# Kernel optimization log

Measured on AMD Instinct MI355X. Metric: run time of the kernel, lower is better.

Reference implementation:

```python
import jax, jax.numpy as jnp
import numpy as np

N_NODES = 100000
N_EDGES = 1600000
IN_C = 128
HID_C = 128   # 2 * out_channels
OUT_C = 64


def gcn_conv(x, row, col, w, W, b, num_nodes):
    """PyG GCNConv: linear transform, add self-loops (weight 1),
    symmetric degree normalization, scatter-sum aggregation, bias."""
    h = x @ W  # [N, C_out]
    loop = jnp.arange(num_nodes, dtype=row.dtype)
    r = jnp.concatenate([row, loop])
    c = jnp.concatenate([col, loop])
    ew = jnp.concatenate([w, jnp.ones((num_nodes,), dtype=w.dtype)])
    deg = jax.ops.segment_sum(ew, c, num_segments=num_nodes)
    dinv = jnp.where(deg > 0, jax.lax.rsqrt(deg), 0.0)
    norm = dinv[r] * ew * dinv[c]            # [E+N]
    msg = h[r] * norm[:, None]               # [E+N, C_out] gather
    out = jax.ops.segment_sum(msg, c, num_segments=num_nodes)
    return out + b


def setup_inputs() -> dict:
    key = jax.random.key(0)
    k1, k2, k3, k4, k5, k6, k7, k8 = jax.random.split(key, 8)
    x = jax.random.normal(k1, (N_NODES, IN_C), dtype=jnp.float32)
    edge_index = jax.random.randint(k2, (2, N_EDGES), 0, N_NODES, dtype=jnp.int64)
    edge_weight = jax.random.uniform(k3, (N_EDGES,), dtype=jnp.float32)
    s1 = float(np.sqrt(6.0 / (IN_C + HID_C)))
    s2 = float(np.sqrt(6.0 / (HID_C + OUT_C)))
    W1 = jax.random.uniform(k4, (IN_C, HID_C), minval=-s1, maxval=s1, dtype=jnp.float32)
    b1 = jnp.zeros((HID_C,), dtype=jnp.float32)
    W2 = jax.random.uniform(k5, (HID_C, OUT_C), minval=-s2, maxval=s2, dtype=jnp.float32)
    b2 = jnp.zeros((OUT_C,), dtype=jnp.float32)
    return {"x": x, "edge_index": edge_index, "edge_weight": edge_weight,
            "W1": W1, "b1": b1, "W2": W2, "b2": b2}


def reference(x, edge_index, edge_weight, W1, b1, W2, b2):
    row, col = edge_index[0], edge_index[1]
    n = x.shape[0]
    h = jax.nn.relu(gcn_conv(x, row, col, edge_weight, W1, b1, n))
    h = jax.nn.relu(gcn_conv(h, row, col, edge_weight, W2, b2, n))
    return h
```

## Files before the change

kernel.cpp:

```cpp
#include <hip/hip_runtime.h>

#define TPB 256

typedef unsigned int uint32;
typedef unsigned short ushort_t;
typedef __attribute__((ext_vector_type(8))) short bf16x8;
typedef __attribute__((ext_vector_type(4))) float f32x4;

constexpr int NB = 256;
constexpr int B1 = 256;

__device__ __forceinline__ uint32 pack_bf16x2(float a, float b) {
  uint32 ua = __float_as_uint(a), ub = __float_as_uint(b);
  ua += 0x7FFFu + ((ua >> 16) & 1u);
  ub += 0x7FFFu + ((ub >> 16) & 1u);
  return (ua >> 16) | (ub & 0xFFFF0000u);
}
__device__ __forceinline__ ushort_t bf16_of(float a) {
  uint32 u = __float_as_uint(a);
  u += 0x7FFFu + ((u >> 16) & 1u);
  return (ushort_t)(u >> 16);
}
__device__ __forceinline__ float bf16_lo(uint32 u) { return __uint_as_float(u << 16); }
__device__ __forceinline__ float bf16_hi(uint32 u) { return __uint_as_float(u & 0xFFFF0000u); }

__global__ __launch_bounds__(256) void rx_hist(const int* __restrict__ col,
                                               int* __restrict__ blockhist, int e, int chunk) {
  __shared__ int h[NB];
  int tid = threadIdx.x, blk = blockIdx.x;
  h[tid] = 0;
  __syncthreads();
  int s = blk * chunk, t = min(e, s + chunk);
  for (int i = s + tid; i < t; i += 256) atomicAdd(&h[col[i] & 255], 1);
  __syncthreads();
  blockhist[tid * B1 + blk] = h[tid];
}

__global__ __launch_bounds__(256) void k_scan1(int* __restrict__ a, int* __restrict__ bsum, int n) {
  __shared__ int s[256];
  int tid = threadIdx.x;
  int base = blockIdx.x * 1024 + tid * 4;
  int v0 = 0, v1 = 0, v2 = 0, v3 = 0;
  if (base + 0 < n) v0 = a[base + 0];
  if (base + 1 < n) v1 = a[base + 1];
  if (base + 2 < n) v2 = a[base + 2];
  if (base + 3 < n) v3 = a[base + 3];
  int tsum = v0 + v1 + v2 + v3;
  s[tid] = tsum;
  __syncthreads();
  for (int off = 1; off < 256; off <<= 1) {
    int t = (tid >= off) ? s[tid - off] : 0;
    __syncthreads();
    s[tid] += t;
    __syncthreads();
  }
  if (tid == 255) bsum[blockIdx.x] = s[255];
  int e0 = s[tid] - tsum;
  int e1 = e0 + v0, e2 = e1 + v1, e3 = e2 + v2;
  if (base + 0 < n) a[base + 0] = e0;
  if (base + 1 < n) a[base + 1] = e1;
  if (base + 2 < n) a[base + 2] = e2;
  if (base + 3 < n) a[base + 3] = e3;
}

__global__ __launch_bounds__(256) void k_scan2(int* __restrict__ bsum, int nb) {
  __shared__ int s[256];
  int tid = threadIdx.x;
  int v = (tid < nb) ? bsum[tid] : 0;
  s[tid] = v;
  __syncthreads();
  for (int off = 1; off < 256; off <<= 1) {
    int t = (tid >= off) ? s[tid - off] : 0;
    __syncthreads();
    s[tid] += t;
    __syncthreads();
  }
  if (tid < nb) bsum[tid] = s[tid] - v;
}

__global__ void k_scan3b(int* __restrict__ a, const int* __restrict__ bsum, int n) {
  int i = blockIdx.x * TPB + threadIdx.x;
  if (i < n) a[i] += bsum[i >> 10];
}

__global__ __launch_bounds__(256) void rx_scatter1(const int* __restrict__ row,
                                                   const int* __restrict__ col,
                                                   const float* __restrict__ w,
                                                   const int* __restrict__ scanned,
                                                   int2* __restrict__ rec, int e, int chunk) {
  __shared__ int cur[NB];
  int tid = threadIdx.x, blk = blockIdx.x;
  cur[tid] = scanned[tid * B1 + blk];
  __syncthreads();
  int s = blk * chunk, t = min(e, s + chunk);
  for (int i = s + tid; i < t; i += 256) {
    int c = col[i];
    int p = atomicAdd(&cur[c & 255], 1);
    rec[p] = make_int2(row[i] | ((c >> 8) << 20), __float_as_int(w[i]));
  }
}

__global__ __launch_bounds__(256) void rx_build(const int2* __restrict__ rec,
                                                const int* __restrict__ scanned,
                                                int2* __restrict__ nodeRange,
                                                float* __restrict__ dinv,
                                                int2* __restrict__ edges, int n, int e) {
  constexpr int NH = 512;
  __shared__ int cnt[NH];
  __shared__ int pref[NH];
  __shared__ int cur[NH];
  __shared__ float dw[NH];
  __shared__ int ssum[256];
  int tid = threadIdx.x, lo = blockIdx.x;
  int s = scanned[lo * B1];
  int t = (lo == NB - 1) ? e : scanned[(lo + 1) * B1];
  cnt[tid] = 0; cnt[tid + 256] = 0;
  dw[tid] = 0.f; dw[tid + 256] = 0.f;
  __syncthreads();
  for (int i = s + tid; i < t; i += 256) {
    int2 r = rec[i];
    int hi = ((uint32)r.x) >> 20;
    atomicAdd(&cnt[hi], 1);
    atomicAdd(&dw[hi], __int_as_float(r.y));
  }
  __syncthreads();
  int a0 = cnt[2 * tid], a1 = cnt[2 * tid + 1];
  int sum2 = a0 + a1;
  ssum[tid] = sum2;
  __syncthreads();
  for (int off = 1; off < 256; off <<= 1) {
    int v = (tid >= off) ? ssum[tid - off] : 0;
    __syncthreads();
    ssum[tid] += v;
    __syncthreads();
  }
  int excl = ssum[tid] - sum2;
  pref[2 * tid] = excl;
  pref[2 * tid + 1] = excl + a0;
  __syncthreads();
#pragma unroll
  for (int k = 0; k < 2; ++k) {
    int hi = tid + k * 256;
    int node = (hi << 8) | lo;
    cur[hi] = s + pref[hi];
    if (node < n) {
      nodeRange[node] = make_int2(s + pref[hi], cnt[hi]);
      dinv[node] = rsqrtf(1.0f + dw[hi]);
    }
  }
  __syncthreads();
  for (int i = s + tid; i < t; i += 256) {
    int2 r = rec[i];
    int hi = ((uint32)r.x) >> 20;
    int p = atomicAdd(&cur[hi], 1);
    edges[p] = make_int2(r.x & 0xFFFFF, r.y);
  }
}

__global__ void k_wprep2(const float* __restrict__ W1, ushort_t* __restrict__ Wt1,
                         const float* __restrict__ W2, ushort_t* __restrict__ Wt2) {
  int i = blockIdx.x * TPB + threadIdx.x;
  if (i < 128 * 128) {
    int k = i >> 7, m = i & 127;
    Wt1[m * 128 + k] = bf16_of(W1[i]);
  } else {
    int j = i - 128 * 128;
    if (j < 128 * 64) {
      int k = j >> 6, m = j & 63;
      Wt2[m * 128 + k] = bf16_of(W2[j]);
    }
  }
}

template <int M, bool XF32>
__global__ __launch_bounds__(256) void k_gemm_mfma(
    const void* __restrict__ Xv, const ushort_t* __restrict__ Wt,
    const float* __restrict__ dinv, uint32* __restrict__ Hb, int n) {
  __shared__ __align__(16) char smem[16384 + M * 256];
  char* Xs = smem;
  char* Ws = smem + 16384;
  const int tid = threadIdx.x;
  const int lane = tid & 63;
  const int w = tid >> 6;
  const int row0 = blockIdx.x * 64;

  {
    const uint4* src = (const uint4*)Wt;
    for (int idx = tid; idx < M * 16; idx += 256) {
      int r = idx >> 4, g = idx & 15;
      uint4 v = src[idx];
      *(uint4*)(Ws + ((r << 8) | ((g << 4) ^ ((r & 7) << 4)))) = v;
    }
  }
  if constexpr (XF32) {
    const float4* src = (const float4*)Xv;
    for (int idx = tid; idx < 64 * 16; idx += 256) {
      int r = idx >> 4, g = idx & 15;
      int grow = row0 + r;
      float4 va = make_float4(0.f, 0.f, 0.f, 0.f), vb = va;
      if (grow < n) {
        va = src[(size_t)grow * 32 + g * 2];
        vb = src[(size_t)grow * 32 + g * 2 + 1];
      }
      uint4 p;
      p.x = pack_bf16x2(va.x, va.y);
      p.y = pack_bf16x2(va.z, va.w);
      p.z = pack_bf16x2(vb.x, vb.y);
      p.w = pack_bf16x2(vb.z, vb.w);
      *(uint4*)(Xs + ((r << 8) | ((g << 4) ^ ((r & 7) << 4)))) = p;
    }
  } else {
    const uint4* src = (const uint4*)Xv;
    for (int idx = tid; idx < 64 * 16; idx += 256) {
      int r = idx >> 4, g = idx & 15;
      int grow = row0 + r;
      uint4 v = make_uint4(0u, 0u, 0u, 0u);
      if (grow < n) v = src[(size_t)grow * 16 + g];
      *(uint4*)(Xs + ((r << 8) | ((g << 4) ^ ((r & 7) << 4)))) = v;
    }
  }
  __syncthreads();

  constexpr int CT = M / 16;
  f32x4 acc[CT];
#pragma unroll
  for (int c = 0; c < CT; ++c) acc[c] = (f32x4){0.f, 0.f, 0.f, 0.f};

  const int arow = (w << 4) | (lane & 15);
  const int kb0 = (lane >> 4) << 4;
#pragma unroll
  for (int ks = 0; ks < 4; ++ks) {
    int kbyte = ks * 64 + kb0;
    bf16x8 a = *(const bf16x8*)(Xs + ((arow << 8) | (kbyte ^ ((arow & 7) << 4))));
#pragma unroll
    for (int c = 0; c < CT; ++c) {
      int brow = c * 16 + (lane & 15);
      bf16x8 b = *(const bf16x8*)(Ws + ((brow << 8) | (kbyte ^ ((brow & 7) << 4))));
      acc[c] = __builtin_amdgcn_mfma_f32_16x16x32_bf16(a, b, acc[c], 0, 0, 0);
    }
  }
  __syncthreads();

  ushort_t* Cs = (ushort_t*)smem;
  const int rbase = (w << 4) | ((lane >> 4) << 2);
  float dv[4];
#pragma unroll
  for (int r = 0; r < 4; ++r) {
    int g = row0 + rbase + r;
    dv[r] = (g < n) ? dinv[g] : 0.f;
  }
#pragma unroll
  for (int c = 0; c < CT; ++c) {
    int col = c * 16 + (lane & 15);
#pragma unroll
    for (int r = 0; r < 4; ++r)
      Cs[(rbase + r) * 132 + col] = bf16_of(acc[c][r] * dv[r]);
  }
  __syncthreads();
  constexpr int G2 = M / 4;
  uint2* dst = (uint2*)Hb;
  for (int idx = tid; idx < 64 * G2; idx += 256) {
    int r = idx / G2, g = idx % G2;
    int grow = row0 + r;
    if (grow < n)
      dst[(size_t)grow * G2 + g] = *(const uint2*)((const char*)Cs + r * 264 + g * 8);
  }
}

template <int C>
__global__ __launch_bounds__(TPB) void k_agg(
    const uint32* __restrict__ hsb, const int2* __restrict__ edges,
    const int2* __restrict__ nodeRange, const float* __restrict__ dinv,
    const float* __restrict__ bias, void* __restrict__ out, int n) {
  int node = (blockIdx.x * TPB + threadIdx.x) >> 6;
  if (node >= n) return;
  int lane = threadIdx.x & 63;
  int g = lane >> 4;
  int gl = lane & 15;
  int2 nr = nodeRange[node];
  int s0 = nr.x, s1 = nr.x + nr.y;
  float di = dinv[node];

  if constexpr (C == 128) {
    const uint4* h4 = (const uint4*)hsb;
    float a0, a1, a2, a3, a4, a5, a6, a7;
    if (g == 0) {
      uint4 u = h4[(size_t)node * 16 + gl];
      a0 = bf16_lo(u.x); a1 = bf16_hi(u.x); a2 = bf16_lo(u.y); a3 = bf16_hi(u.y);
      a4 = bf16_lo(u.z); a5 = bf16_hi(u.z); a6 = bf16_lo(u.w); a7 = bf16_hi(u.w);
    } else {
      a0 = a1 = a2 = a3 = a4 = a5 = a6 = a7 = 0.f;
    }
    int k = s0 + g;
    for (; k + 4 < s1; k += 8) {
      int2 e0 = edges[k], e1 = edges[k + 4];
      uint4 v0 = h4[(size_t)e0.x * 16 + gl];
      uint4 v1 = h4[(size_t)e1.x * 16 + gl];
      float w0 = __int_as_float(e0.y), w1 = __int_as_float(e1.y);
      a0 = fmaf(bf16_lo(v0.x), w0, a0); a1 = fmaf(bf16_hi(v0.x), w0, a1);
      a2 = fmaf(bf16_lo(v0.y), w0, a2); a3 = fmaf(bf16_hi(v0.y), w0, a3);
      a4 = fmaf(bf16_lo(v0.z), w0, a4); a5 = fmaf(bf16_hi(v0.z), w0, a5);
      a6 = fmaf(bf16_lo(v0.w), w0, a6); a7 = fmaf(bf16_hi(v0.w), w0, a7);
      a0 = fmaf(bf16_lo(v1.x), w1, a0); a1 = fmaf(bf16_hi(v1.x), w1, a1);
      a2 = fmaf(bf16_lo(v1.y), w1, a2); a3 = fmaf(bf16_hi(v1.y), w1, a3);
      a4 = fmaf(bf16_lo(v1.z), w1, a4); a5 = fmaf(bf16_hi(v1.z), w1, a5);
      a6 = fmaf(bf16_lo(v1.w), w1, a6); a7 = fmaf(bf16_hi(v1.w), w1, a7);
    }
    if (k < s1) {
      int2 e0 = edges[k];
      uint4 v0 = h4[(size_t)e0.x * 16 + gl];
      float w0 = __int_as_float(e0.y);
      a0 = fmaf(bf16_lo(v0.x), w0, a0); a1 = fmaf(bf16_hi(v0.x), w0, a1);
      a2 = fmaf(bf16_lo(v0.y), w0, a2); a3 = fmaf(bf16_hi(v0.y), w0, a3);
      a4 = fmaf(bf16_lo(v0.z), w0, a4); a5 = fmaf(bf16_hi(v0.z), w0, a5);
      a6 = fmaf(bf16_lo(v0.w), w0, a6); a7 = fmaf(bf16_hi(v0.w), w0, a7);
    }
    a0 += __shfl_xor(a0, 16); a1 += __shfl_xor(a1, 16);
    a2 += __shfl_xor(a2, 16); a3 += __shfl_xor(a3, 16);
    a4 += __shfl_xor(a4, 16); a5 += __shfl_xor(a5, 16);
    a6 += __shfl_xor(a6, 16); a7 += __shfl_xor(a7, 16);
    a0 += __shfl_xor(a0, 32); a1 += __shfl_xor(a1, 32);
    a2 += __shfl_xor(a2, 32); a3 += __shfl_xor(a3, 32);
    a4 += __shfl_xor(a4, 32); a5 += __shfl_xor(a5, 32);
    a6 += __shfl_xor(a6, 32); a7 += __shfl_xor(a7, 32);
    if (g == 0) {
      float4 bb0 = ((const float4*)bias)[gl * 2];
      float4 bb1 = ((const float4*)bias)[gl * 2 + 1];
      uint4 ob;
      ob.x = pack_bf16x2(fmaxf(fmaf(a0, di, bb0.x), 0.f), fmaxf(fmaf(a1, di, bb0.y), 0.f));
      ob.y = pack_bf16x2(fmaxf(fmaf(a2, di, bb0.z), 0.f), fmaxf(fmaf(a3, di, bb0.w), 0.f));
      ob.z = pack_bf16x2(fmaxf(fmaf(a4, di, bb1.x), 0.f), fmaxf(fmaf(a5, di, bb1.y), 0.f));
      ob.w = pack_bf16x2(fmaxf(fmaf(a6, di, bb1.z), 0.f), fmaxf(fmaf(a7, di, bb1.w), 0.f));
      ((uint4*)out)[(size_t)node * 16 + gl] = ob;
    }
  } else {
    const uint2* h2 = (const uint2*)hsb;
    float a0, a1, a2, a3;
    if (g == 0) {
      uint2 u = h2[(size_t)node * 16 + gl];
      a0 = bf16_lo(u.x); a1 = bf16_hi(u.x); a2 = bf16_lo(u.y); a3 = bf16_hi(u.y);
    } else {
      a0 = a1 = a2 = a3 = 0.f;
    }
    int k = s0 + g;
    for (; k + 4 < s1; k += 8) {
      int2 e0 = edges[k], e1 = edges[k + 4];
      uint2 v0 = h2[(size_t)e0.x * 16 + gl];
      uint2 v1 = h2[(size_t)e1.x * 16 + gl];
      float w0 = __int_as_float(e0.y), w1 = __int_as_float(e1.y);
      a0 = fmaf(bf16_lo(v0.x), w0, a0); a1 = fmaf(bf16_hi(v0.x), w0, a1);
      a2 = fmaf(bf16_lo(v0.y), w0, a2); a3 = fmaf(bf16_hi(v0.y), w0, a3);
      a0 = fmaf(bf16_lo(v1.x), w1, a0); a1 = fmaf(bf16_hi(v1.x), w1, a1);
      a2 = fmaf(bf16_lo(v1.y), w1, a2); a3 = fmaf(bf16_hi(v1.y), w1, a3);
    }
    if (k < s1) {
      int2 e0 = edges[k];
      uint2 v0 = h2[(size_t)e0.x * 16 + gl];
      float w0 = __int_as_float(e0.y);
      a0 = fmaf(bf16_lo(v0.x), w0, a0); a1 = fmaf(bf16_hi(v0.x), w0, a1);
      a2 = fmaf(bf16_lo(v0.y), w0, a2); a3 = fmaf(bf16_hi(v0.y), w0, a3);
    }
    a0 += __shfl_xor(a0, 16); a1 += __shfl_xor(a1, 16);
    a2 += __shfl_xor(a2, 16); a3 += __shfl_xor(a3, 16);
    a0 += __shfl_xor(a0, 32); a1 += __shfl_xor(a1, 32);
    a2 += __shfl_xor(a2, 32); a3 += __shfl_xor(a3, 32);
    if (g == 0) {
      float4 bb = ((const float4*)bias)[gl];
      float4 o;
      o.x = fmaxf(fmaf(a0, di, bb.x), 0.f);
      o.y = fmaxf(fmaf(a1, di, bb.y), 0.f);
      o.z = fmaxf(fmaf(a2, di, bb.z), 0.f);
      o.w = fmaxf(fmaf(a3, di, bb.w), 0.f);
      ((float4*)out)[(size_t)node * 16 + gl] = o;
    }
  }
}

extern "C" void kernel_launch(void* const* d_in, const int* in_sizes, int n_in,
                              void* d_out, int out_size, void* d_ws, size_t ws_size,
                              hipStream_t stream) {
  const float* x  = (const float*)d_in[0];
  const int*   ei = (const int*)d_in[1];
  const float* ew = (const float*)d_in[2];
  const float* W1 = (const float*)d_in[3];
  const float* b1 = (const float*)d_in[4];
  const float* W2 = (const float*)d_in[5];
  const float* b2 = (const float*)d_in[6];
  float* out = (float*)d_out;

  constexpr int IN_C = 128, HID = 128, OUTC = 64;
  const int n = in_sizes[0] / IN_C;
  const int e = in_sizes[2];
  const int* rowp = ei;
  const int* colp = ei + e;

  auto cdiv = [](long a, long b) { return (int)((a + b - 1) / b); };
  auto align = [](size_t v) { return (v + 255) & ~(size_t)255; };

  char* ws = (char*)d_ws;
  size_t o = 0;
  int*      blockhist = (int*)(ws + o);     o = align(o + (size_t)NB * B1 * 4);
  int*      bsum      = (int*)(ws + o);     o = align(o + 4096);
  float*    dinv      = (float*)(ws + o);   o = align(o + (size_t)n * 4);
  int2*     nodeRange = (int2*)(ws + o);    o = align(o + (size_t)n * 8);
  ushort_t* Wt1       = (ushort_t*)(ws + o); o = align(o + (size_t)HID * IN_C * 2);
  ushort_t* Wt2       = (ushort_t*)(ws + o); o = align(o + (size_t)OUTC * HID * 2);
  int2*     rec       = (int2*)(ws + o);    o = align(o + (size_t)e * 8);
  int2*     edges     = (int2*)(ws + o);    o = align(o + (size_t)e * 8);
  uint32*   hs1b      = (uint32*)(ws + o);  o = align(o + (size_t)n * (HID / 2) * 4);
  uint32*   o1b       = (uint32*)(ws + o);  o = align(o + (size_t)n * (HID / 2) * 4);
  uint32*   hs2b      = hs1b;

  const int chunk = cdiv(e, B1);
  const int nscan = NB * B1;

  rx_hist<<<B1, 256, 0, stream>>>(colp, blockhist, e, chunk);
  k_wprep2<<<cdiv(IN_C * HID + HID * OUTC, TPB), TPB, 0, stream>>>(W1, Wt1, W2, Wt2);
  k_scan1<<<nscan / 1024, 256, 0, stream>>>(blockhist, bsum, nscan);
  k_scan2<<<1, 256, 0, stream>>>(bsum, nscan / 1024);
  k_scan3b<<<nscan / TPB, TPB, 0, stream>>>(blockhist, bsum, nscan);
  rx_scatter1<<<B1, 256, 0, stream>>>(rowp, colp, ew, blockhist, rec, e, chunk);
  rx_build<<<NB, 256, 0, stream>>>(rec, blockhist, nodeRange, dinv, edges, n, e);

  k_gemm_mfma<HID, true><<<cdiv(n, 64), 256, 0, stream>>>(x, Wt1, dinv, hs1b, n);
  k_agg<HID><<<cdiv(n, 4), TPB, 0, stream>>>(hs1b, edges, nodeRange, dinv, b1, o1b, n);

  k_gemm_mfma<OUTC, false><<<cdiv(n, 64), 256, 0, stream>>>(o1b, Wt2, dinv, hs2b, n);
  k_agg<OUTC><<<cdiv(n, 4), TPB, 0, stream>>>(hs2b, edges, nodeRange, dinv, b2, out, n);
}
```

Baseline: 210.2 us.

## Fuse weight prep and scan fixup into neighbors; stage edges in LDS for aggregation

The bf16 weight-transpose work moves into the histogram kernel, and the scan block-offset add is folded into the scatter and build kernels. Together these drop two kernel launches and one full pass over the histogram array. The aggregation kernel now has each wave load up to 64 of its node's edge records into shared memory with one coalesced nontemporal load. It then gathers neighbor features four at a time per lane group, aiming for more memory-level parallelism. Nodes with more than 64 edges fall back to reading the remaining edge records from global memory.

```diff
diff --git a/kernel.cpp b/kernel.cpp
--- a/kernel.cpp
+++ b/kernel.cpp
@@ -25,13 +25,24 @@
 __device__ __forceinline__ float bf16_hi(uint32 u) { return __uint_as_float(u & 0xFFFF0000u); }
 
 __global__ __launch_bounds__(256) void rx_hist(const int* __restrict__ col,
-                                               int* __restrict__ blockhist, int e, int chunk) {
+                                               int* __restrict__ blockhist, int e, int chunk,
+                                               const float* __restrict__ W1, ushort_t* __restrict__ Wt1,
+                                               const float* __restrict__ W2, ushort_t* __restrict__ Wt2) {
   __shared__ int h[NB];
   int tid = threadIdx.x, blk = blockIdx.x;
   h[tid] = 0;
   __syncthreads();
   int s = blk * chunk, t = min(e, s + chunk);
   for (int i = s + tid; i < t; i += 256) atomicAdd(&h[col[i] & 255], 1);
+  int gtid = blk * 256 + tid;
+  if (gtid < 128 * 128) {
+    int k = gtid >> 7, m = gtid & 127;
+    Wt1[m * 128 + k] = bf16_of(W1[gtid]);
+  } else if (gtid < 128 * 128 + 128 * 64) {
+    int j = gtid - 128 * 128;
+    int k = j >> 6, m = j & 63;
+    Wt2[m * 128 + k] = bf16_of(W2[j]);
+  }
   __syncthreads();
   blockhist[tid * B1 + blk] = h[tid];
 }
@@ -78,19 +89,16 @@
   if (tid < nb) bsum[tid] = s[tid] - v;
 }
 
-__global__ void k_scan3b(int* __restrict__ a, const int* __restrict__ bsum, int n) {
-  int i = blockIdx.x * TPB + threadIdx.x;
-  if (i < n) a[i] += bsum[i >> 10];
-}
-
 __global__ __launch_bounds__(256) void rx_scatter1(const int* __restrict__ row,
                                                    const int* __restrict__ col,
                                                    const float* __restrict__ w,
                                                    const int* __restrict__ scanned,
+                                                   const int* __restrict__ bsum,
                                                    int2* __restrict__ rec, int e, int chunk) {
   __shared__ int cur[NB];
   int tid = threadIdx.x, blk = blockIdx.x;
-  cur[tid] = scanned[tid * B1 + blk];
+  int idx = tid * B1 + blk;
+  cur[tid] = scanned[idx] + bsum[idx >> 10];
   __syncthreads();
   int s = blk * chunk, t = min(e, s + chunk);
   for (int i = s + tid; i < t; i += 256) {
@@ -102,6 +110,7 @@
 
 __global__ __launch_bounds__(256) void rx_build(const int2* __restrict__ rec,
                                                 const int* __restrict__ scanned,
+                                                const int* __restrict__ bsum,
                                                 int2* __restrict__ nodeRange,
                                                 float* __restrict__ dinv,
                                                 int2* __restrict__ edges, int n, int e) {
@@ -112,8 +121,14 @@
   __shared__ float dw[NH];
   __shared__ int ssum[256];
   int tid = threadIdx.x, lo = blockIdx.x;
-  int s = scanned[lo * B1];
-  int t = (lo == NB - 1) ? e : scanned[(lo + 1) * B1];
+  int si = lo * B1;
+  int s = scanned[si] + bsum[si >> 10];
+  int t;
+  if (lo == NB - 1) t = e;
+  else {
+    int ti = (lo + 1) * B1;
+    t = scanned[ti] + bsum[ti >> 10];
+  }
   cnt[tid] = 0; cnt[tid + 256] = 0;
   dw[tid] = 0.f; dw[tid + 256] = 0.f;
   __syncthreads();
@@ -154,21 +169,6 @@
     int hi = ((uint32)r.x) >> 20;
     int p = atomicAdd(&cur[hi], 1);
     edges[p] = make_int2(r.x & 0xFFFFF, r.y);
-  }
-}
-
-__global__ void k_wprep2(const float* __restrict__ W1, ushort_t* __restrict__ Wt1,
-                         const float* __restrict__ W2, ushort_t* __restrict__ Wt2) {
-  int i = blockIdx.x * TPB + threadIdx.x;
-  if (i < 128 * 128) {
-    int k = i >> 7, m = i & 127;
-    Wt1[m * 128 + k] = bf16_of(W1[i]);
-  } else {
-    int j = i - 128 * 128;
-    if (j < 128 * 64) {
-      int k = j >> 6, m = j & 63;
-      Wt2[m * 128 + k] = bf16_of(W2[j]);
-    }
   }
 }
 
@@ -272,14 +272,22 @@
     const uint32* __restrict__ hsb, const int2* __restrict__ edges,
     const int2* __restrict__ nodeRange, const float* __restrict__ dinv,
     const float* __restrict__ bias, void* __restrict__ out, int n) {
+  __shared__ int2 ebuf[TPB / 64][64];
   int node = (blockIdx.x * TPB + threadIdx.x) >> 6;
   if (node >= n) return;
   int lane = threadIdx.x & 63;
+  int wv = (threadIdx.x >> 6) & (TPB / 64 - 1);
   int g = lane >> 4;
   int gl = lane & 15;
   int2 nr = nodeRange[node];
-  int s0 = nr.x, s1 = nr.x + nr.y;
+  int s0 = nr.x, cnt = nr.y;
+  int nLds = min(cnt, 64);
   float di = dinv[node];
+
+  if (lane < nLds) {
+    long long ev = __builtin_nontemporal_load((const long long*)(edges + s0 + lane));
+    ebuf[wv][lane] = make_int2((int)ev, (int)(ev >> 32));
+  }
 
   if constexpr (C == 128) {
     const uint4* h4 = (const uint4*)hsb;
@@ -291,12 +299,15 @@
     } else {
       a0 = a1 = a2 = a3 = a4 = a5 = a6 = a7 = 0.f;
     }
-    int k = s0 + g;
-    for (; k + 4 < s1; k += 8) {
-      int2 e0 = edges[k], e1 = edges[k + 4];
+    int k = g;
+    for (; k + 12 < nLds; k += 16) {
+      int2 e0 = ebuf[wv][k], e1 = ebuf[wv][k + 4], e2 = ebuf[wv][k + 8], e3 = ebuf[wv][k + 12];
       uint4 v0 = h4[(size_t)e0.x * 16 + gl];
       uint4 v1 = h4[(size_t)e1.x * 16 + gl];
+      uint4 v2 = h4[(size_t)e2.x * 16 + gl];
+      uint4 v3 = h4[(size_t)e3.x * 16 + gl];
       float w0 = __int_as_float(e0.y), w1 = __int_as_float(e1.y);
+      float w2 = __int_as_float(e2.y), w3 = __int_as_float(e3.y);
       a0 = fmaf(bf16_lo(v0.x), w0, a0); a1 = fmaf(bf16_hi(v0.x), w0, a1);
       a2 = fmaf(bf16_lo(v0.y), w0, a2); a3 = fmaf(bf16_hi(v0.y), w0, a3);
       a4 = fmaf(bf16_lo(v0.z), w0, a4); a5 = fmaf(bf16_hi(v0.z), w0, a5);
@@ -305,9 +316,26 @@
       a2 = fmaf(bf16_lo(v1.y), w1, a2); a3 = fmaf(bf16_hi(v1.y), w1, a3);
       a4 = fmaf(bf16_lo(v1.z), w1, a4); a5 = fmaf(bf16_hi(v1.z), w1, a5);
       a6 = fmaf(bf16_lo(v1.w), w1, a6); a7 = fmaf(bf16_hi(v1.w), w1, a7);
-    }
-    if (k < s1) {
-      int2 e0 = edges[k];
+      a0 = fmaf(bf16_lo(v2.x), w2, a0); a1 = fmaf(bf16_hi(v2.x), w2, a1);
+      a2 = fmaf(bf16_lo(v2.y), w2, a2); a3 = fmaf(bf16_hi(v2.y), w2, a3);
+      a4 = fmaf(bf16_lo(v2.z), w2, a4); a5 = fmaf(bf16_hi(v2.z), w2, a5);
+      a6 = fmaf(bf16_lo(v2.w), w2, a6); a7 = fmaf(bf16_hi(v2.w), w2, a7);
+      a0 = fmaf(bf16_lo(v3.x), w3, a0); a1 = fmaf(bf16_hi(v3.x), w3, a1);
+      a2 = fmaf(bf16_lo(v3.y), w3, a2); a3 = fmaf(bf16_hi(v3.y), w3, a3);
+      a4 = fmaf(bf16_lo(v3.z), w3, a4); a5 = fmaf(bf16_hi(v3.z), w3, a5);
+      a6 = fmaf(bf16_lo(v3.w), w3, a6); a7 = fmaf(bf16_hi(v3.w), w3, a7);
+    }
+    for (; k < nLds; k += 4) {
+      int2 e0 = ebuf[wv][k];
+      uint4 v0 = h4[(size_t)e0.x * 16 + gl];
+      float w0 = __int_as_float(e0.y);
+      a0 = fmaf(bf16_lo(v0.x), w0, a0); a1 = fmaf(bf16_hi(v0.x), w0, a1);
+      a2 = fmaf(bf16_lo(v0.y), w0, a2); a3 = fmaf(bf16_hi(v0.y), w0, a3);
+      a4 = fmaf(bf16_lo(v0.z), w0, a4); a5 = fmaf(bf16_hi(v0.z), w0, a5);
+      a6 = fmaf(bf16_lo(v0.w), w0, a6); a7 = fmaf(bf16_hi(v0.w), w0, a7);
+    }
+    for (int kk = s0 + 64 + g; kk < s0 + cnt; kk += 4) {
+      int2 e0 = edges[kk];
       uint4 v0 = h4[(size_t)e0.x * 16 + gl];
       float w0 = __int_as_float(e0.y);
       a0 = fmaf(bf16_lo(v0.x), w0, a0); a1 = fmaf(bf16_hi(v0.x), w0, a1);
@@ -342,19 +370,33 @@
     } else {
       a0 = a1 = a2 = a3 = 0.f;
     }
-    int k = s0 + g;
-    for (; k + 4 < s1; k += 8) {
-      int2 e0 = edges[k], e1 = edges[k + 4];
+    int k = g;
+    for (; k + 12 < nLds; k += 16) {
+      int2 e0 = ebuf[wv][k], e1 = ebuf[wv][k + 4], e2 = ebuf[wv][k + 8], e3 = ebuf[wv][k + 12];
       uint2 v0 = h2[(size_t)e0.x * 16 + gl];
       uint2 v1 = h2[(size_t)e1.x * 16 + gl];
+      uint2 v2 = h2[(size_t)e2.x * 16 + gl];
+      uint2 v3 = h2[(size_t)e3.x * 16 + gl];
       float w0 = __int_as_float(e0.y), w1 = __int_as_float(e1.y);
+      float w2 = __int_as_float(e2.y), w3 = __int_as_float(e3.y);
       a0 = fmaf(bf16_lo(v0.x), w0, a0); a1 = fmaf(bf16_hi(v0.x), w0, a1);
       a2 = fmaf(bf16_lo(v0.y), w0, a2); a3 = fmaf(bf16_hi(v0.y), w0, a3);
       a0 = fmaf(bf16_lo(v1.x), w1, a0); a1 = fmaf(bf16_hi(v1.x), w1, a1);
       a2 = fmaf(bf16_lo(v1.y), w1, a2); a3 = fmaf(bf16_hi(v1.y), w1, a3);
-    }
-    if (k < s1) {
-      int2 e0 = edges[k];
+      a0 = fmaf(bf16_lo(v2.x), w2, a0); a1 = fmaf(bf16_hi(v2.x), w2, a1);
+      a2 = fmaf(bf16_lo(v2.y), w2, a2); a3 = fmaf(bf16_hi(v2.y), w2, a3);
+      a0 = fmaf(bf16_lo(v3.x), w3, a0); a1 = fmaf(bf16_hi(v3.x), w3, a1);
+      a2 = fmaf(bf16_lo(v3.y), w3, a2); a3 = fmaf(bf16_hi(v3.y), w3, a3);
+    }
+    for (; k < nLds; k += 4) {
+      int2 e0 = ebuf[wv][k];
+      uint2 v0 = h2[(size_t)e0.x * 16 + gl];
+      float w0 = __int_as_float(e0.y);
+      a0 = fmaf(bf16_lo(v0.x), w0, a0); a1 = fmaf(bf16_hi(v0.x), w0, a1);
+      a2 = fmaf(bf16_lo(v0.y), w0, a2); a3 = fmaf(bf16_hi(v0.y), w0, a3);
+    }
+    for (int kk = s0 + 64 + g; kk < s0 + cnt; kk += 4) {
+      int2 e0 = edges[kk];
       uint2 v0 = h2[(size_t)e0.x * 16 + gl];
       float w0 = __int_as_float(e0.y);
       a0 = fmaf(bf16_lo(v0.x), w0, a0); a1 = fmaf(bf16_hi(v0.x), w0, a1);
@@ -414,13 +456,11 @@
   const int chunk = cdiv(e, B1);
   const int nscan = NB * B1;
 
-  rx_hist<<<B1, 256, 0, stream>>>(colp, blockhist, e, chunk);
-  k_wprep2<<<cdiv(IN_C * HID + HID * OUTC, TPB), TPB, 0, stream>>>(W1, Wt1, W2, Wt2);
+  rx_hist<<<B1, 256, 0, stream>>>(colp, blockhist, e, chunk, W1, Wt1, W2, Wt2);
   k_scan1<<<nscan / 1024, 256, 0, stream>>>(blockhist, bsum, nscan);
   k_scan2<<<1, 256, 0, stream>>>(bsum, nscan / 1024);
-  k_scan3b<<<nscan / TPB, TPB, 0, stream>>>(blockhist, bsum, nscan);
-  rx_scatter1<<<B1, 256, 0, stream>>>(rowp, colp, ew, blockhist, rec, e, chunk);
-  rx_build<<<NB, 256, 0, stream>>>(rec, blockhist, nodeRange, dinv, edges, n, e);
+  rx_scatter1<<<B1, 256, 0, stream>>>(rowp, colp, ew, blockhist, bsum, rec, e, chunk);
+  rx_build<<<NB, 256, 0, stream>>>(rec, blockhist, bsum, nodeRange, dinv, edges, n, e);
 
   k_gemm_mfma<HID, true><<<cdiv(n, 64), 256, 0, stream>>>(x, Wt1, dinv, hs1b, n);
   k_agg<HID><<<cdiv(n, 4), TPB, 0, stream>>>(hs1b, edges, nodeRange, dinv, b1, o1b, n);
```

After: 210.2 us. About the same (-0.0%).
